# Performance work log

Hardware: AMD Instinct MI355X
Metric: run time of the kernel (lower is better)

The kernel has to match this reference:

```python
import jax, jax.numpy as jnp
import numpy as np

B, L, D = 128, 196, 512
T = 20
V, E, H, A = 10000, 256, 512, 512


def setup_inputs() -> dict:
    key = jax.random.key(0)
    ks = jax.random.split(key, 20)
    s = lambda *sh: 0.02
    inp = {
        "a": jax.random.normal(ks[0], (B, L, D), jnp.float32),
        "captions": jax.random.randint(ks[1], (B, T), 0, V),
        "lengths": jnp.full((B,), T, dtype=jnp.int64),
        "embed_W": jax.random.normal(ks[2], (V, E), jnp.float32) * 0.02,
        "Wa": jax.random.normal(ks[3], (D, A), jnp.float32) * 0.02,
        "Wh": jax.random.normal(ks[4], (H, A), jnp.float32) * 0.02,
        "Wc": jax.random.normal(ks[5], (H, A), jnp.float32) * 0.02,
        "v": jax.random.normal(ks[6], (A,), jnp.float32) * 0.02,
        "beta_W": jax.random.normal(ks[7], (H, 1), jnp.float32) * 0.02,
        "beta_b": jnp.zeros((1,), jnp.float32),
        "W_ih": jax.random.normal(ks[8], (E + D, 4 * H), jnp.float32) * 0.02,
        "W_hh": jax.random.normal(ks[9], (H, 4 * H), jnp.float32) * 0.02,
        "b_ih": jnp.zeros((4 * H,), jnp.float32),
        "b_hh": jnp.zeros((4 * H,), jnp.float32),
        "fc_W": jax.random.normal(ks[10], (H, V), jnp.float32) * 0.02,
        "fc_b": jnp.zeros((V,), jnp.float32),
        "initW_h": jax.random.normal(ks[11], (D, H), jnp.float32) * 0.02,
        "initb_h": jnp.zeros((H,), jnp.float32),
        "initW_c": jax.random.normal(ks[12], (D, H), jnp.float32) * 0.02,
        "initb_c": jnp.zeros((H,), jnp.float32),
    }
    return inp


def _decode(a, captions, embed_W, Wa, Wh, Wc, v, beta_W, beta_b,
            W_ih, W_hh, b_ih, b_hh, fc_W, fc_b,
            initW_h, initb_h, initW_c, initb_c):
    # dropout layers are treated as identity (eval mode) for a deterministic reference
    emb = embed_W[captions]                       # (B, T, E)
    mean_ctx = a.mean(axis=1)                     # (B, D)
    h0 = jnp.tanh(mean_ctx @ initW_h + initb_h)   # (B, H)
    c0 = jnp.tanh(mean_ctx @ initW_c + initb_c)
    wa = a @ Wa                                   # (B, L, A), hoisted (invariant over t)
    Hd = h0.shape[-1]

    def step(carry, x_t):
        h, c, prev_h = carry
        # dual additive attention: scores from annotations + h + prev_h (context_input)
        score = jnp.tanh(wa + (h @ Wh)[:, None, :] + (prev_h @ Wc)[:, None, :])  # (B,L,A)
        e = score @ v                                                            # (B,L)
        alpha = jax.nn.softmax(e, axis=1)
        beta = jax.nn.sigmoid(h @ beta_W + beta_b)                               # (B,1)
        ctx = beta * jnp.einsum('bl,bld->bd', alpha, a)                          # (B,D)
        # LSTMCell
        x = jnp.concatenate([x_t, ctx], axis=1)                                  # (B,E+D)
        gates = x @ W_ih + b_ih + h @ W_hh + b_hh                                # (B,4H)
        i, f, g, o = jnp.split(gates, 4, axis=1)
        c_new = jax.nn.sigmoid(f) * c + jax.nn.sigmoid(i) * jnp.tanh(g)
        h_new = jax.nn.sigmoid(o) * jnp.tanh(c_new)
        logits_t = h_new @ fc_W + fc_b                                           # (B,V)
        return (h_new, c_new, h_new), (logits_t, alpha)

    xs = jnp.swapaxes(emb[:, :T - 1, :], 0, 1)    # (T-1, B, E) time-major
    _, (logits_t, alphas_t) = jax.lax.scan(step, (h0, c0, h0), xs)
    # all lengths == T: pack_padded_sequence(batch_first=True).data is time-major flatten
    packed_logits = logits_t.reshape((T - 1) * a.shape[0], -1)                   # ((T-1)*B, V)
    alphas = jnp.swapaxes(alphas_t, 0, 1)                                        # (B, T-1, L)
    return packed_logits, alphas


def reference(a, captions, lengths, embed_W, Wa, Wh, Wc, v, beta_W, beta_b,
              W_ih, W_hh, b_ih, b_hh, fc_W, fc_b,
              initW_h, initb_h, initW_c, initb_c):
    return _decode(a, captions, embed_W, Wa, Wh, Wc, v, beta_W, beta_b,
                   W_ih, W_hh, b_ih, b_hh, fc_W, fc_b,
                   initW_h, initb_h, initW_c, initb_c)
```

## Files before the change

### kernel.cpp

```cpp
#include <hip/hip_runtime.h>
#include <hip/hip_bf16.h>
#include <math.h>

#define B_ 128
#define L_ 196
#define D_ 512
#define T_ 20
#define V_ 10000
#define E_ 256
#define H_ 512
#define A_ 512
#define TM1 19
#define ROWS (TM1*B_)
#define G4H 2048
#define KCAT 1024
#define LH 98

typedef unsigned short ushort_t;
typedef __attribute__((ext_vector_type(8))) short bf16x8;
typedef __attribute__((ext_vector_type(4))) float f32x4;

__device__ __forceinline__ float fast_tanh(float x){
    float ax = fabsf(x);
    float e = __expf(-2.f*ax);
    float r = __builtin_amdgcn_rcpf(1.f + e);
    return copysignf((1.f - e)*r, x);
}
__device__ __forceinline__ float sigmoidf_(float x){
    return __builtin_amdgcn_rcpf(1.f + __expf(-x));
}
__device__ __forceinline__ ushort_t f2b(float f){
    union{float f; unsigned u;} x; x.f = f;
    unsigned r = x.u + 0x7fffu + ((x.u>>16)&1u);
    return (ushort_t)(r>>16);
}
__device__ __forceinline__ float b2f(ushort_t h){
    union{unsigned u; float f;} x; x.u = ((unsigned)h)<<16;
    return x.f;
}
__device__ __forceinline__ float b2f_lo(unsigned u){ union{unsigned u; float f;} x; x.u = u<<16; return x.f; }
__device__ __forceinline__ float b2f_hi(unsigned u){ union{unsigned u; float f;} x; x.u = u & 0xffff0000u; return x.f; }

#define GL16(gsrc, ldst) __builtin_amdgcn_global_load_lds( \
    (const __attribute__((address_space(1))) unsigned*)(gsrc), \
    (__attribute__((address_space(3))) unsigned*)(ldst), 16, 0, 0)

template<int OUT_BF16, int HAS_BIAS, int NT, int SWZ>
__global__ __launch_bounds__(256)
void gemm_mfma(const ushort_t* __restrict__ A, int lda,
               const ushort_t* __restrict__ BT, int ldb,
               void* __restrict__ Cout, int ldc,
               int N, int K, const float* __restrict__ bias)
{
    __shared__ ushort_t As[2][4096];
    __shared__ ushort_t Bs[2][4096];
    int bm, bn;
    if (SWZ){
        int bid = blockIdx.x;
        int swz = (bid & 7)*190 + (bid >> 3);
        int mt = swz % 19, nt = swz / 19;
        if (nt >= 79) return;
        bm = mt*128; bn = nt*128;
    } else {
        bm = blockIdx.y * 128; bn = blockIdx.x * 128;
    }
    const int tid = threadIdx.x;
    const int lane = tid & 63;
    const int wave = tid >> 6;
    const int wm = (wave >> 1) * 64;
    const int wn = (wave & 1) * 64;
    const int lrow = lane & 15;
    const int lk8  = (lane >> 4) * 8;
    const int srow = tid >> 2;
    const int skq0 = (tid & 3) * 8;
    const int wbase = wave * 512;

    f32x4 acc[4][4];
    #pragma unroll
    for (int i=0;i<4;i++)
        #pragma unroll
        for (int j=0;j<4;j++) acc[i][j] = (f32x4){0.f,0.f,0.f,0.f};

    const ushort_t* Ab = A  + (size_t)(bm+srow)*lda + skq0;
    const ushort_t* Bb = BT + (size_t)(bn+srow)*ldb + skq0;

    GL16(Ab,                    &As[0][wbase]);
    GL16(Ab + (size_t)64*lda,   &As[0][2048 + wbase]);
    GL16(Bb,                    &Bs[0][wbase]);
    GL16(Bb + (size_t)64*ldb,   &Bs[0][2048 + wbase]);

    int buf = 0;
    for (int k0 = 0; k0 < K; k0 += 32) {
        asm volatile("s_waitcnt vmcnt(0)" ::: "memory");
        __syncthreads();
        if (k0 + 32 < K){
            int nb = buf ^ 1;
            GL16(Ab + k0 + 32,                  &As[nb][wbase]);
            GL16(Ab + (size_t)64*lda + k0 + 32, &As[nb][2048 + wbase]);
            GL16(Bb + k0 + 32,                  &Bs[nb][wbase]);
            GL16(Bb + (size_t)64*ldb + k0 + 32, &Bs[nb][2048 + wbase]);
        }
        bf16x8 af[4], bfr[4];
        #pragma unroll
        for (int i=0;i<4;i++) af[i]  = *(bf16x8*)&As[buf][(wm + i*16 + lrow)*32 + lk8];
        #pragma unroll
        for (int j=0;j<4;j++) bfr[j] = *(bf16x8*)&Bs[buf][(wn + j*16 + lrow)*32 + lk8];
        #pragma unroll
        for (int i=0;i<4;i++)
            #pragma unroll
            for (int j=0;j<4;j++)
                acc[i][j] = __builtin_amdgcn_mfma_f32_16x16x32_bf16(af[i], bfr[j], acc[i][j], 0, 0, 0);
        buf ^= 1;
    }

    const int rq = (lane >> 4) * 4;
    #pragma unroll
    for (int j=0;j<4;j++){
        int col = bn + wn + j*16 + lrow;
        if (col >= N) continue;
        float bv = HAS_BIAS ? bias[col] : 0.f;
        #pragma unroll
        for (int i=0;i<4;i++){
            #pragma unroll
            for (int q=0;q<4;q++){
                int row = bm + wm + i*16 + rq + q;
                float v = acc[i][j][q] + bv;
                if (OUT_BF16) ((ushort_t*)Cout)[(size_t)row*ldc + col] = f2b(v);
                else if (NT)  __builtin_nontemporal_store(v, &((float*)Cout)[(size_t)row*ldc + col]);
                else          ((float*)Cout)[(size_t)row*ldc + col] = v;
            }
        }
    }
}

struct GJob { const ushort_t* A; int lda; const ushort_t* BT; int ldb;
              void* C; int ldc; int N, K; const float* bias; int out_bf16; int nx; int nblk; };

__global__ __launch_bounds__(256) void gemm_dual_k(GJob j0, GJob j1){
    __shared__ ushort_t As[2][4096];
    __shared__ ushort_t Bs[2][4096];
    int bid = blockIdx.x;
    GJob jb = (bid < j0.nblk) ? j0 : j1;
    if (bid >= j0.nblk) bid -= j0.nblk;
    const int bn = (bid % jb.nx)*128, bm = (bid / jb.nx)*128;
    const int tid = threadIdx.x;
    const int lane = tid & 63;
    const int wave = tid >> 6;
    const int wm = (wave >> 1) * 64;
    const int wn = (wave & 1) * 64;
    const int lrow = lane & 15;
    const int lk8  = (lane >> 4) * 8;
    const int srow = tid >> 2;
    const int skq0 = (tid & 3) * 8;
    const int wbase = wave * 512;

    f32x4 acc[4][4];
    #pragma unroll
    for (int i=0;i<4;i++)
        #pragma unroll
        for (int j=0;j<4;j++) acc[i][j] = (f32x4){0.f,0.f,0.f,0.f};

    const ushort_t* Ab = jb.A  + (size_t)(bm+srow)*jb.lda + skq0;
    const ushort_t* Bb = jb.BT + (size_t)(bn+srow)*jb.ldb + skq0;

    GL16(Ab,                        &As[0][wbase]);
    GL16(Ab + (size_t)64*jb.lda,    &As[0][2048 + wbase]);
    GL16(Bb,                        &Bs[0][wbase]);
    GL16(Bb + (size_t)64*jb.ldb,    &Bs[0][2048 + wbase]);

    int buf = 0;
    for (int k0 = 0; k0 < jb.K; k0 += 32) {
        asm volatile("s_waitcnt vmcnt(0)" ::: "memory");
        __syncthreads();
        if (k0 + 32 < jb.K){
            int nb = buf ^ 1;
            GL16(Ab + k0 + 32,                      &As[nb][wbase]);
            GL16(Ab + (size_t)64*jb.lda + k0 + 32,  &As[nb][2048 + wbase]);
            GL16(Bb + k0 + 32,                      &Bs[nb][wbase]);
            GL16(Bb + (size_t)64*jb.ldb + k0 + 32,  &Bs[nb][2048 + wbase]);
        }
        bf16x8 af[4], bfr[4];
        #pragma unroll
        for (int i=0;i<4;i++) af[i]  = *(bf16x8*)&As[buf][(wm + i*16 + lrow)*32 + lk8];
        #pragma unroll
        for (int j=0;j<4;j++) bfr[j] = *(bf16x8*)&Bs[buf][(wn + j*16 + lrow)*32 + lk8];
        #pragma unroll
        for (int i=0;i<4;i++)
            #pragma unroll
            for (int j=0;j<4;j++)
                acc[i][j] = __builtin_amdgcn_mfma_f32_16x16x32_bf16(af[i], bfr[j], acc[i][j], 0, 0, 0);
        buf ^= 1;
    }

    const int rq = (lane >> 4) * 4;
    #pragma unroll
    for (int j=0;j<4;j++){
        int col = bn + wn + j*16 + lrow;
        if (col >= jb.N) continue;
        float bv = jb.bias ? jb.bias[col] : 0.f;
        #pragma unroll
        for (int i=0;i<4;i++){
            #pragma unroll
            for (int q=0;q<4;q++){
                int row = bm + wm + i*16 + rq + q;
                float v = acc[i][j][q] + bv;
                if (jb.out_bf16) ((ushort_t*)jb.C)[(size_t)row*jb.ldc + col] = f2b(v);
                else             ((float*)jb.C)[(size_t)row*jb.ldc + col] = v;
            }
        }
    }
}

__global__ __launch_bounds__(256) void gemm64t2(const float* __restrict__ Amcp, int lda,
                       const float* __restrict__ B0, const float* __restrict__ B1, int ldb,
                       float* __restrict__ C0, float* __restrict__ C1, int ldc,
                       const float* __restrict__ bias0, const float* __restrict__ bias1)
{
    const float* Bm  = blockIdx.z ? B1 : B0;
    float* C         = blockIdx.z ? C1 : C0;
    const float* bias= blockIdx.z ? bias1 : bias0;
    __shared__ float As[16][65];
    __shared__ float Bs[16][65];
    int bm = blockIdx.y*64, bn = blockIdx.x*64;
    int tid = threadIdx.x;
    int tx = tid & 15, ty = tid >> 4;
    const float invL = 1.f/(float)L_;
    float acc[4][4] = {};
    for (int k0 = 0; k0 < D_; k0 += 16) {
        {
            int r  = tid >> 2;
            int kq = (tid & 3) * 4;
            const float* Ap = Amcp + (size_t)(bm+r)*lda + k0 + kq;
            float4 v0 = *(const float4*)(Ap);
            float4 v1 = *(const float4*)(Ap + 65536);
            float4 v2 = *(const float4*)(Ap + 131072);
            float4 v3 = *(const float4*)(Ap + 196608);
            float4 va = make_float4((v0.x+v1.x+v2.x+v3.x)*invL, (v0.y+v1.y+v2.y+v3.y)*invL,
                                    (v0.z+v1.z+v2.z+v3.z)*invL, (v0.w+v1.w+v2.w+v3.w)*invL);
            As[kq+0][r]=va.x; As[kq+1][r]=va.y; As[kq+2][r]=va.z; As[kq+3][r]=va.w;
        }
        {
            int kk = tid >> 4;
            int nq = (tid & 15) * 4;
            float4 vb = *(const float4*)(Bm + (size_t)(k0+kk)*ldb + bn + nq);
            Bs[kk][nq+0]=vb.x; Bs[kk][nq+1]=vb.y; Bs[kk][nq+2]=vb.z; Bs[kk][nq+3]=vb.w;
        }
        __syncthreads();
        #pragma unroll
        for (int k = 0; k < 16; ++k) {
            float a0[4], b0[4];
            #pragma unroll
            for (int i=0;i<4;i++) a0[i] = As[k][ty*4+i];
            #pragma unroll
            for (int j=0;j<4;j++) b0[j] = Bs[k][tx*4+j];
            #pragma unroll
            for (int i=0;i<4;i++)
                #pragma unroll
                for (int j=0;j<4;j++)
                    acc[i][j] = fmaf(a0[i], b0[j], acc[i][j]);
        }
        __syncthreads();
    }
    #pragma unroll
    for (int i=0;i<4;i++){
        int row = bm + ty*4 + i;
        #pragma unroll
        for (int j=0;j<4;j++){
            int col = bn + tx*4 + j;
            C[(size_t)row*ldc + col] = fast_tanh(acc[i][j] + bias[col]);
        }
    }
}

struct TJob { const float* src; const float* src2; ushort_t* dst;
              int lds, Ksz, Nsz, koff, ldk, nx, nblk; };
struct PrepArgs {
    TJob j[6];
    const float* a; ushort_t* a_b; float* mcp;
    const float* b_ih; const float* b_hh; float* bias4h; unsigned* ebar;
    const int* caps; const float* embW; ushort_t* xemb;
};

__global__ __launch_bounds__(256) void prep_all_k(PrepArgs P){
    __shared__ float t[32][33];
    int bid = blockIdx.x;
    const int tid = threadIdx.x;
    if (bid < 256){
        const int b = bid >> 1, half = bid & 1;
        const int quad = tid & 127;
        const int sl = tid >> 7;
        const int pi = half*2 + sl;
        const int l0 = half*LH + sl*49;
        const float* p = P.a + ((size_t)(b*L_ + l0))*D_ + quad*4;
        ushort_t* q = P.a_b + ((size_t)(b*L_ + l0))*D_ + quad*4;
        float4 s = make_float4(0.f,0.f,0.f,0.f);
        for (int l=0;l<49;l++){
            float4 v = *(const float4*)(p + (size_t)l*D_);
            s.x += v.x; s.y += v.y; s.z += v.z; s.w += v.w;
            ushort_t r[4] = {f2b(v.x),f2b(v.y),f2b(v.z),f2b(v.w)};
            *(uint2*)(q + (size_t)l*D_) = *(uint2*)r;
        }
        *(float4*)(P.mcp + (size_t)pi*65536 + (size_t)b*D_ + quad*4) = s;
        return;
    }
    bid -= 256;
    if (bid < 8128){
        int ji = 0;
        while (bid >= P.j[ji].nblk){ bid -= P.j[ji].nblk; ji++; }
        const TJob jb = P.j[ji];
        int n0 = (bid % jb.nx)*32, k0 = (bid / jb.nx)*32;
        int tx = tid & 31, ty = tid >> 5;
        #pragma unroll
        for (int kk = ty; kk < 32; kk += 8){
            int k = k0 + kk, n = n0 + tx;
            float v = 0.f;
            if (k < jb.Ksz && n < jb.Nsz){
                v = jb.src[(size_t)k*jb.lds + n];
                if (jb.src2) v += jb.src2[(size_t)k*jb.lds + n];
            }
            t[kk][tx] = v;
        }
        __syncthreads();
        #pragma unroll
        for (int nn = ty; nn < 32; nn += 8){
            int n = n0 + nn, k = k0 + tx;
            if (k < jb.Ksz) jb.dst[(size_t)n*jb.ldk + jb.koff + k] = f2b(t[tx][nn]);
        }
        return;
    }
    bid -= 8128;
    if (bid == 0){
        for (int k = tid; k < G4H; k += 256) P.bias4h[k] = P.b_ih[k] + P.b_hh[k];
        if (tid < B_) P.ebar[tid] = 0u;
        return;
    }
    bid -= 1;
    int i = bid*4 + (tid >> 6);
    int lane = tid & 63;
    int tt = i / B_, b = i - tt*B_;
    int cap = P.caps[b*T_ + tt];
    float4 v = ((const float4*)(P.embW + (size_t)cap*E_))[lane];
    ushort_t r[4] = {f2b(v.x),f2b(v.y),f2b(v.z),f2b(v.w)};
    *(uint2*)(P.xemb + (size_t)i*E_ + lane*4) = *(uint2*)r;
}

__global__ __launch_bounds__(512) void hw0cvt_k(const float* __restrict__ h0f,
                        const ushort_t* __restrict__ WhcT, const float* __restrict__ beta_W,
                        ushort_t* __restrict__ xcat, float* __restrict__ hWp, float* __restrict__ bdot){
    int b = blockIdx.x, tid = threadIdx.x;
    int lane = tid & 63, wave = tid >> 6;
    __shared__ ushort_t hls[512];
    __shared__ float rr[8];
    float hv = h0f[b*H_ + tid];
    ushort_t hb = f2b(hv);
    xcat[(size_t)b*KCAT + D_ + tid] = hb;
    hls[tid] = hb;
    hWp[(size_t)(b*2+1)*512 + tid] = 0.f;
    float dv = hv * beta_W[tid];
    #pragma unroll
    for (int off=32; off; off>>=1) dv += __shfl_down(dv, off);
    if (lane==0) rr[wave] = dv;
    __syncthreads();
    if (tid == 0){
        float s = rr[0]+rr[1]+rr[2]+rr[3]+rr[4]+rr[5]+rr[6]+rr[7];
        bdot[b*2] = s; bdot[b*2+1] = 0.f;
    }
    int wn = wave * 64;
    int col16 = lane & 15;
    int khi = (lane >> 4) * 8;
    bool a_on = (col16 == 0);
    f32x4 acc[4];
    #pragma unroll
    for (int f=0;f<4;f++) acc[f] = (f32x4){0.f,0.f,0.f,0.f};
    for (int kk=0; kk<16; kk++){
        bf16x8 af = (bf16x8){0,0,0,0,0,0,0,0};
        if (a_on) af = *(const bf16x8*)&hls[kk*32 + khi];
        #pragma unroll
        for (int f=0;f<4;f++){
            bf16x8 bf = *(const bf16x8*)(WhcT + (size_t)(wn + f*16 + col16)*512 + kk*32 + khi);
            acc[f] = __builtin_amdgcn_mfma_f32_16x16x32_bf16(af, bf, acc[f], 0, 0, 0);
        }
    }
    if (lane < 16){
        #pragma unroll
        for (int f=0;f<4;f++) hWp[(size_t)(b*2+0)*512 + wn + f*16 + lane] = acc[f][0];
    }
}

__global__ __launch_bounds__(512) void mega2_k(const ushort_t* __restrict__ wa,
                        const ushort_t* __restrict__ a_b,
                        const float* __restrict__ v,
                        const float* __restrict__ beta_W, const float* __restrict__ beta_b,
                        const ushort_t* __restrict__ WhcT,
                        const float* __restrict__ gp, const float* __restrict__ embWih,
                        float* __restrict__ cbuf, float* __restrict__ hWp,
                        ushort_t* __restrict__ xcat, ushort_t* __restrict__ Hall,
                        float* __restrict__ alphas_out, float* __restrict__ ebuf,
                        unsigned* __restrict__ ebar, float* __restrict__ bdot, int t)
{
    const int b = blockIdx.x, half = blockIdx.y;
    const int tid = threadIdx.x;
    const int lane = tid & 63, wave = tid >> 6;
    __shared__ ushort_t hls[256];
    __shared__ float red[16];
    __shared__ float al_s[224];
    __shared__ float4 part4[8][64];

    if (t > 0){
        float dv = 0.f;
        if (tid < 256){
            const int j = half*256 + tid;
            const float* eb = embWih + ((size_t)((t-1)*B_ + b))*G4H;
            float gi = eb[j], gf = eb[H_+j], gg = eb[2*H_+j], go = eb[3*H_+j];
            #pragma unroll
            for (int ks=0; ks<8; ks++){
                const float* g = gp + ((size_t)(ks*B_ + b))*G4H;
                gi += g[j]; gf += g[H_+j]; gg += g[2*H_+j]; go += g[3*H_+j];
            }
            float ig = sigmoidf_(gi), fg = sigmoidf_(gf);
            float g2 = fast_tanh(gg), og = sigmoidf_(go);
            float c = fg*cbuf[b*H_+j] + ig*g2;
            float h = og*fast_tanh(c);
            cbuf[b*H_+j] = c;
            ushort_t hb = f2b(h);
            xcat[(size_t)b*KCAT + D_ + j] = hb;
            Hall[((size_t)(t-1)*B_ + b)*H_ + j] = hb;
            hls[tid] = hb;
            dv = h * beta_W[j];
        }
        #pragma unroll
        for (int off=32; off; off>>=1) dv += __shfl_down(dv, off);
        if (lane==0) red[wave] = dv;
        __syncthreads();
        int wn = wave * 64;
        int col16 = lane & 15;
        int khi = (lane >> 4) * 8;
        bool a_on = (col16 == 0);
        f32x4 acc[4];
        #pragma unroll
        for (int f=0;f<4;f++) acc[f] = (f32x4){0.f,0.f,0.f,0.f};
        #pragma unroll
        for (int kk=0; kk<8; kk++){
            bf16x8 af = (bf16x8){0,0,0,0,0,0,0,0};
            if (a_on) af = *(const bf16x8*)&hls[kk*32 + khi];
            #pragma unroll
            for (int f=0;f<4;f++){
                bf16x8 bf = *(const bf16x8*)(WhcT + (size_t)(wn + f*16 + col16)*512 + half*256 + kk*32 + khi);
                acc[f] = __builtin_amdgcn_mfma_f32_16x16x32_bf16(af, bf, acc[f], 0, 0, 0);
            }
        }
        if (lane < 16){
            #pragma unroll
            for (int f=0;f<4;f++) hWp[(size_t)(b*2+half)*512 + wn + f*16 + lane] = acc[f][0];
        }
    }
    __syncthreads();
    if (tid == 0){
        if (t > 0) bdot[b*2+half] = red[0]+red[1]+red[2]+red[3];
        __threadfence();
        atomicAdd(&ebar[b], 1u);
        const unsigned tgt = 2u*(unsigned)(2*t+1);
        while (__hip_atomic_load(&ebar[b], __ATOMIC_ACQUIRE, __HIP_MEMORY_SCOPE_AGENT) < tgt)
            __builtin_amdgcn_s_sleep(1);
    }
    __syncthreads();
    {
        const float* hp0 = hWp + (size_t)(b*2+0)*512 + lane*8;
        const float* hp1 = hWp + (size_t)(b*2+1)*512 + lane*8;
        float4 p00 = *(const float4*)hp0, p01 = *(const float4*)(hp0+4);
        float4 p10 = *(const float4*)hp1, p11 = *(const float4*)(hp1+4);
        float4 hw0 = make_float4(p00.x+p10.x, p00.y+p10.y, p00.z+p10.z, p00.w+p10.w);
        float4 hw1 = make_float4(p01.x+p11.x, p01.y+p11.y, p01.z+p11.z, p01.w+p11.w);
        const float* vp = v + lane*8;
        float4 v0 = *(const float4*)vp, v1 = *(const float4*)(vp+4);
        const int l0 = half*LH;
        for (int r = wave; r < LH; r += 8){
            int4 raw = *(const int4*)(wa + (((size_t)(b*L_ + l0 + r))<<9) + lane*8);
            const unsigned* u = (const unsigned*)&raw;
            float s;
            s  = fast_tanh(b2f_lo(u[0]) + hw0.x)*v0.x;
            s += fast_tanh(b2f_hi(u[0]) + hw0.y)*v0.y;
            s += fast_tanh(b2f_lo(u[1]) + hw0.z)*v0.z;
            s += fast_tanh(b2f_hi(u[1]) + hw0.w)*v0.w;
            s += fast_tanh(b2f_lo(u[2]) + hw1.x)*v1.x;
            s += fast_tanh(b2f_hi(u[2]) + hw1.y)*v1.y;
            s += fast_tanh(b2f_lo(u[3]) + hw1.z)*v1.z;
            s += fast_tanh(b2f_hi(u[3]) + hw1.w)*v1.w;
            #pragma unroll
            for (int off=32; off; off>>=1) s += __shfl_down(s, off);
            if (lane==0) ebuf[b*L_ + l0 + r] = s;
        }
    }
    __syncthreads();
    if (tid == 0){
        __threadfence();
        atomicAdd(&ebar[b], 1u);
        const unsigned tgt = 2u*(unsigned)(2*t+2);
        while (__hip_atomic_load(&ebar[b], __ATOMIC_ACQUIRE, __HIP_MEMORY_SCOPE_AGENT) < tgt)
            __builtin_amdgcn_s_sleep(1);
    }
    __syncthreads();
    float ev = (tid < L_) ? ebuf[b*L_ + tid] : -3.0e38f;
    float wmax = ev;
    #pragma unroll
    for (int off=32; off; off>>=1) wmax = fmaxf(wmax, __shfl_down(wmax, off));
    if (lane==0) red[wave] = wmax;
    __syncthreads();
    float m = fmaxf(fmaxf(fmaxf(red[0],red[1]),fmaxf(red[2],red[3])),
                    fmaxf(fmaxf(red[4],red[5]),fmaxf(red[6],red[7])));
    float pr = (tid < L_) ? __expf(ev - m) : 0.f;
    float wsum = pr;
    #pragma unroll
    for (int off=32; off; off>>=1) wsum += __shfl_down(wsum, off);
    if (lane==0) red[8+wave] = wsum;
    __syncthreads();
    float inv = 1.f / (red[8]+red[9]+red[10]+red[11]+red[12]+red[13]+red[14]+red[15]);
    if (tid < L_) al_s[tid] = pr*inv;
    const int l0 = half*LH;
    if (tid >= l0 && tid < l0 + LH)
        __builtin_nontemporal_store(pr*inv, alphas_out + (size_t)b*TM1*L_ + (size_t)t*L_ + tid);
    __syncthreads();
    {
        const int dg = tid & 63;
        const int lr = tid >> 6;
        const int d0 = half*256 + dg*4;
        const ushort_t* pa = a_b + (((size_t)(b*L_))<<9) + d0;
        float4 s = make_float4(0.f,0.f,0.f,0.f);
        for (int l = lr; l < L_; l += 8){
            uint2 av = *(const uint2*)(pa + ((size_t)l<<9));
            float al = al_s[l];
            s.x = fmaf(al, b2f_lo(av.x), s.x);
            s.y = fmaf(al, b2f_hi(av.x), s.y);
            s.z = fmaf(al, b2f_lo(av.y), s.z);
            s.w = fmaf(al, b2f_hi(av.y), s.w);
        }
        part4[lr][dg] = s;
        __syncthreads();
        if (tid < 64){
            float beta = sigmoidf_(bdot[b*2] + bdot[b*2+1] + beta_b[0]);
            float4 r = make_float4(0.f,0.f,0.f,0.f);
            #pragma unroll
            for (int q=0;q<8;q++){
                float4 pv = part4[q][tid];
                r.x += pv.x; r.y += pv.y; r.z += pv.z; r.w += pv.w;
            }
            unsigned lo = (unsigned)f2b(beta*r.x) | (((unsigned)f2b(beta*r.y))<<16);
            unsigned hi = (unsigned)f2b(beta*r.z) | (((unsigned)f2b(beta*r.w))<<16);
            uint2 pk; pk.x = lo; pk.y = hi;
            *(uint2*)(xcat + (size_t)b*KCAT + half*256 + tid*4) = pk;
        }
    }
}

__global__ __launch_bounds__(256) void gates_k(const ushort_t* __restrict__ xcat,
                        const ushort_t* __restrict__ WcatT, float* __restrict__ gp){
    __shared__ ushort_t As[128*32];
    __shared__ ushort_t Bs[64*32];
    const int bn = blockIdx.x*64;
    const int ks = blockIdx.y;
    const int tid = threadIdx.x;
    const int lane = tid & 63, wave = tid >> 6;
    const int wm = wave*32;
    const int lrow = lane & 15;
    const int lk8 = (lane >> 4) * 8;
    f32x4 acc[2][4];
    #pragma unroll
    for (int i=0;i<2;i++)
        #pragma unroll
        for (int j=0;j<4;j++) acc[i][j] = (f32x4){0.f,0.f,0.f,0.f};

    for (int kk = 0; kk < 4; ++kk){
        int k0 = ks*128 + kk*32;
        int c0 = 2*tid;
        int r0 = c0 >> 2,  kq0 = (c0 & 3)*8;
        int r1 = (c0+1) >> 2, kq1 = ((c0+1) & 3)*8;
        int4 a0 = *(const int4*)(xcat + (size_t)r0*KCAT + k0 + kq0);
        int4 a1 = *(const int4*)(xcat + (size_t)r1*KCAT + k0 + kq1);
        int rb = tid >> 2, kqb = (tid & 3)*8;
        int4 b0 = *(const int4*)(WcatT + (size_t)(bn+rb)*KCAT + k0 + kqb);
        __syncthreads();
        *(int4*)&As[r0*32 + kq0] = a0;
        *(int4*)&As[r1*32 + kq1] = a1;
        *(int4*)&Bs[rb*32 + kqb] = b0;
        __syncthreads();
        bf16x8 af[2], bfr[4];
        #pragma unroll
        for (int i=0;i<2;i++) af[i] = *(bf16x8*)&As[(wm + i*16 + lrow)*32 + lk8];
        #pragma unroll
        for (int j=0;j<4;j++) bfr[j] = *(bf16x8*)&Bs[(j*16 + lrow)*32 + lk8];
        #pragma unroll
        for (int i=0;i<2;i++)
            #pragma unroll
            for (int j=0;j<4;j++)
                acc[i][j] = __builtin_amdgcn_mfma_f32_16x16x32_bf16(af[i], bfr[j], acc[i][j], 0, 0, 0);
    }
    const int rq = (lane >> 4) * 4;
    #pragma unroll
    for (int i=0;i<2;i++){
        #pragma unroll
        for (int j=0;j<4;j++){
            int gcol = bn + j*16 + lrow;
            #pragma unroll
            for (int q=0;q<4;q++){
                int grow = wm + i*16 + rq + q;
                gp[((size_t)(ks*B_ + grow))*G4H + gcol] = acc[i][j][q];
            }
        }
    }
}

__global__ __launch_bounds__(512) void lstmfin_k(const float* __restrict__ gp, const float* __restrict__ embWih,
                       const float* __restrict__ cbuf, ushort_t* __restrict__ Hall){
    int b = blockIdx.x, j = threadIdx.x;
    const float* eb = embWih + ((size_t)(18*B_ + b))*G4H;
    float gi = eb[j], gf = eb[H_+j], gg = eb[2*H_+j], go = eb[3*H_+j];
    #pragma unroll
    for (int ks=0; ks<8; ks++){
        const float* g = gp + ((size_t)(ks*B_ + b))*G4H;
        gi += g[j]; gf += g[H_+j]; gg += g[2*H_+j]; go += g[3*H_+j];
    }
    float ig = sigmoidf_(gi), fg = sigmoidf_(gf);
    float g2 = fast_tanh(gg), og = sigmoidf_(go);
    float c = fg*cbuf[b*H_+j] + ig*g2;
    float h = og*fast_tanh(c);
    Hall[((size_t)18*B_ + b)*H_ + j] = f2b(h);
}

extern "C" void kernel_launch(void* const* d_in, const int* in_sizes, int n_in,
                              void* d_out, int out_size, void* d_ws, size_t ws_size,
                              hipStream_t stream) {
    const float* a      = (const float*)d_in[0];
    const int*   caps   = (const int*)  d_in[1];
    const float* embW   = (const float*)d_in[3];
    const float* Wa     = (const float*)d_in[4];
    const float* Wh     = (const float*)d_in[5];
    const float* Wc     = (const float*)d_in[6];
    const float* v      = (const float*)d_in[7];
    const float* beta_W = (const float*)d_in[8];
    const float* beta_b = (const float*)d_in[9];
    const float* W_ih   = (const float*)d_in[10];
    const float* W_hh   = (const float*)d_in[11];
    const float* b_ih   = (const float*)d_in[12];
    const float* b_hh   = (const float*)d_in[13];
    const float* fc_W   = (const float*)d_in[14];
    const float* fc_b   = (const float*)d_in[15];
    const float* iWh    = (const float*)d_in[16];
    const float* ibh    = (const float*)d_in[17];
    const float* iWc    = (const float*)d_in[18];
    const float* ibc    = (const float*)d_in[19];

    float* out    = (float*)d_out;
    float* alphas = out + (size_t)ROWS*V_;

    char* ob = (char*)d_out;
    ushort_t* wa_b   = (ushort_t*)(ob);
    ushort_t* a_b    = (ushort_t*)(ob + 25690112);
    float*    embWih = (float*)   (ob + 51380224);

    char* wb = (char*)d_ws;
    float* mcp      = (float*)(wb);
    float* bdot     = (float*)(wb + 1048576);
    float* cbuf     = (float*)(wb + 1052672);
    float* h0f      = (float*)(wb + 1314816);
    float* hWp      = (float*)(wb + 1576960);
    float* ebuf     = (float*)(wb + 2101248);
    float* bias4h   = (float*)(wb + 2203648);
    unsigned* ebar  = (unsigned*)(wb + 2211840);
    float* gp       = (float*)(wb + 2215936);
    ushort_t* xcat_b = (ushort_t*)(wb + 10604544);
    ushort_t* xemb_b = (ushort_t*)(wb + 10866688);
    ushort_t* Hall   = (ushort_t*)(wb + 12111872);
    ushort_t* WaT    = (ushort_t*)(wb + 14602240);
    ushort_t* WhcT   = (ushort_t*)(wb + 15126528);
    ushort_t* WihT   = (ushort_t*)(wb + 15650816);
    ushort_t* WcatT  = (ushort_t*)(wb + 16699392);
    ushort_t* fcWT   = (ushort_t*)(wb + 20893696);

    PrepArgs P;
    P.j[0] = { Wa,   nullptr, WaT,  512, 512, 512,  0,   512,  16, 256 };
    P.j[1] = { Wh,   Wc,      WhcT, 512, 512, 512,  0,   512,  16, 256 };
    P.j[2] = { W_ih, nullptr, WihT, G4H, 256, G4H,  0,   256,  64, 512 };
    P.j[3] = { W_ih + (size_t)E_*G4H, nullptr, WcatT, G4H, 512, G4H, 0,   KCAT, 64, 1024 };
    P.j[4] = { W_hh, nullptr, WcatT, G4H, 512, G4H,  512, KCAT, 64, 1024 };
    P.j[5] = { fc_W, nullptr, fcWT, V_,  512, V_,   0,   512,  316, 5056 };
    P.a = a; P.a_b = a_b; P.mcp = mcp;
    P.b_ih = b_ih; P.b_hh = b_hh; P.bias4h = bias4h; P.ebar = ebar;
    P.caps = caps; P.embW = embW; P.xemb = xemb_b;
    prep_all_k<<<8993, 256, 0, stream>>>(P);

    gemm64t2<<<dim3(8,2,2), 256, 0, stream>>>(mcp, D_, iWh, iWc, H_, h0f, cbuf, H_, ibh, ibc);
    hw0cvt_k<<<B_, 512, 0, stream>>>(h0f, WhcT, beta_W, xcat_b, hWp, bdot);

    GJob g0 = { a_b,    512, WaT,  512, wa_b,   512, 512,  512, nullptr, 1, 4,  784 };
    GJob g1 = { xemb_b, 256, WihT, 256, embWih, G4H, G4H,  256, bias4h,  0, 16, 304 };
    gemm_dual_k<<<1088, 256, 0, stream>>>(g0, g1);

    for (int t = 0; t < TM1; ++t){
        mega2_k<<<dim3(B_,2), 512, 0, stream>>>(wa_b, a_b, v, beta_W, beta_b, WhcT,
                                                gp, embWih, cbuf, hWp, xcat_b, Hall,
                                                alphas, ebuf, ebar, bdot, t);
        gates_k<<<dim3(32,8), 256, 0, stream>>>(xcat_b, WcatT, gp);
    }
    lstmfin_k<<<B_, 512, 0, stream>>>(gp, embWih, cbuf, Hall);

    gemm_mfma<0,1,1,1><<<dim3(1520), 256, 0, stream>>>(Hall, H_, fcWT, H_, out, V_, V_, H_, fc_b);
}
```

Measured before the change: 1.062 ms.

## Fuse gates GEMM into per-step attention kernel via grid-wide barrier

Merges the per-timestep gates GEMM into the attention/LSTM kernel. A software grid barrier (an atomic counter on a global word plus spin-wait) lets all 256 blocks finish writing xcat before any block computes its gates tile. This removes 19 kernel launches and their launch gaps, and reuses the same blocks for the GEMM with a reworked wave tiling. It relies on all 256 blocks being co-resident, otherwise the spin-wait deadlocks, and it adds LDS usage to the fused kernel.

```diff
diff --git a/kernel.cpp b/kernel.cpp
--- a/kernel.cpp
+++ b/kernel.cpp
@@ -277,7 +277,7 @@
 struct PrepArgs {
     TJob j[6];
     const float* a; ushort_t* a_b; float* mcp;
-    const float* b_ih; const float* b_hh; float* bias4h; unsigned* ebar;
+    const float* b_ih; const float* b_hh; float* bias4h; unsigned* bars;
     const int* caps; const float* embW; ushort_t* xemb;
 };
 
@@ -331,7 +331,7 @@
     bid -= 8128;
     if (bid == 0){
         for (int k = tid; k < G4H; k += 256) P.bias4h[k] = P.b_ih[k] + P.b_hh[k];
-        if (tid < B_) P.ebar[tid] = 0u;
+        P.bars[tid] = 0u;
         return;
     }
     bid -= 1;
@@ -387,24 +387,29 @@
     }
 }
 
-__global__ __launch_bounds__(512) void mega2_k(const ushort_t* __restrict__ wa,
+__global__ __launch_bounds__(512) void mega_k(const ushort_t* __restrict__ wa,
                         const ushort_t* __restrict__ a_b,
                         const float* __restrict__ v,
                         const float* __restrict__ beta_W, const float* __restrict__ beta_b,
-                        const ushort_t* __restrict__ WhcT,
-                        const float* __restrict__ gp, const float* __restrict__ embWih,
+                        const ushort_t* __restrict__ WhcT, const ushort_t* __restrict__ WcatT,
+                        const float* __restrict__ embWih,
                         float* __restrict__ cbuf, float* __restrict__ hWp,
                         ushort_t* __restrict__ xcat, ushort_t* __restrict__ Hall,
                         float* __restrict__ alphas_out, float* __restrict__ ebuf,
-                        unsigned* __restrict__ ebar, float* __restrict__ bdot, int t)
+                        float* __restrict__ gp,
+                        unsigned* __restrict__ ebar, unsigned* __restrict__ gbar,
+                        float* __restrict__ bdot, int t)
 {
-    const int b = blockIdx.x, half = blockIdx.y;
+    const int blk = blockIdx.x;
+    const int b = blk >> 1, half = blk & 1;
     const int tid = threadIdx.x;
     const int lane = tid & 63, wave = tid >> 6;
     __shared__ ushort_t hls[256];
     __shared__ float red[16];
     __shared__ float al_s[224];
     __shared__ float4 part4[8][64];
+    __shared__ ushort_t As[128*32];
+    __shared__ ushort_t Bs[64*32];
 
     if (t > 0){
         float dv = 0.f;
@@ -550,62 +555,60 @@
             *(uint2*)(xcat + (size_t)b*KCAT + half*256 + tid*4) = pk;
         }
     }
-}
-
-__global__ __launch_bounds__(256) void gates_k(const ushort_t* __restrict__ xcat,
-                        const ushort_t* __restrict__ WcatT, float* __restrict__ gp){
-    __shared__ ushort_t As[128*32];
-    __shared__ ushort_t Bs[64*32];
-    const int bn = blockIdx.x*64;
-    const int ks = blockIdx.y;
-    const int tid = threadIdx.x;
-    const int lane = tid & 63, wave = tid >> 6;
-    const int wm = wave*32;
-    const int lrow = lane & 15;
-    const int lk8 = (lane >> 4) * 8;
-    f32x4 acc[2][4];
-    #pragma unroll
-    for (int i=0;i<2;i++)
-        #pragma unroll
-        for (int j=0;j<4;j++) acc[i][j] = (f32x4){0.f,0.f,0.f,0.f};
-
-    for (int kk = 0; kk < 4; ++kk){
-        int k0 = ks*128 + kk*32;
-        int c0 = 2*tid;
-        int r0 = c0 >> 2,  kq0 = (c0 & 3)*8;
-        int r1 = (c0+1) >> 2, kq1 = ((c0+1) & 3)*8;
-        int4 a0 = *(const int4*)(xcat + (size_t)r0*KCAT + k0 + kq0);
-        int4 a1 = *(const int4*)(xcat + (size_t)r1*KCAT + k0 + kq1);
-        int rb = tid >> 2, kqb = (tid & 3)*8;
-        int4 b0 = *(const int4*)(WcatT + (size_t)(bn+rb)*KCAT + k0 + kqb);
-        __syncthreads();
-        *(int4*)&As[r0*32 + kq0] = a0;
-        *(int4*)&As[r1*32 + kq1] = a1;
-        *(int4*)&Bs[rb*32 + kqb] = b0;
-        __syncthreads();
-        bf16x8 af[2], bfr[4];
-        #pragma unroll
-        for (int i=0;i<2;i++) af[i] = *(bf16x8*)&As[(wm + i*16 + lrow)*32 + lk8];
-        #pragma unroll
-        for (int j=0;j<4;j++) bfr[j] = *(bf16x8*)&Bs[(j*16 + lrow)*32 + lk8];
+    __syncthreads();
+    if (tid == 0){
+        __threadfence();
+        atomicAdd(gbar, 1u);
+        const unsigned tgt = 256u*(unsigned)(t+1);
+        while (__hip_atomic_load(gbar, __ATOMIC_ACQUIRE, __HIP_MEMORY_SCOPE_AGENT) < tgt)
+            __builtin_amdgcn_s_sleep(1);
+    }
+    __syncthreads();
+    {
+        const int bn = (blk & 31) * 64;
+        const int ks = blk >> 5;
+        const int wm = (wave & 3) * 32;
+        const int wn = (wave >> 2) * 32;
+        const int lrow = lane & 15, lk8 = (lane >> 4) * 8;
+        const int ra = tid >> 2, kqa = (tid & 3)*8;
+        f32x4 acc[2][2];
         #pragma unroll
         for (int i=0;i<2;i++)
             #pragma unroll
-            for (int j=0;j<4;j++)
-                acc[i][j] = __builtin_amdgcn_mfma_f32_16x16x32_bf16(af[i], bfr[j], acc[i][j], 0, 0, 0);
-    }
-    const int rq = (lane >> 4) * 4;
-    #pragma unroll
-    for (int i=0;i<2;i++){
-        #pragma unroll
-        for (int j=0;j<4;j++){
-            int gcol = bn + j*16 + lrow;
-            #pragma unroll
-            for (int q=0;q<4;q++){
-                int grow = wm + i*16 + rq + q;
-                gp[((size_t)(ks*B_ + grow))*G4H + gcol] = acc[i][j][q];
+            for (int j=0;j<2;j++) acc[i][j] = (f32x4){0.f,0.f,0.f,0.f};
+        #pragma unroll
+        for (int kk = 0; kk < 4; ++kk){
+            int k0 = ks*128 + kk*32;
+            int4 av = *(const int4*)(xcat + (size_t)ra*KCAT + k0 + kqa);
+            int4 bv;
+            if (tid < 256) bv = *(const int4*)(WcatT + (size_t)(bn + ra)*KCAT + k0 + kqa);
+            __syncthreads();
+            *(int4*)&As[ra*32 + kqa] = av;
+            if (tid < 256) *(int4*)&Bs[ra*32 + kqa] = bv;
+            __syncthreads();
+            bf16x8 af[2], bfr[2];
+            #pragma unroll
+            for (int i=0;i<2;i++) af[i]  = *(bf16x8*)&As[(wm + i*16 + lrow)*32 + lk8];
+            #pragma unroll
+            for (int j=0;j<2;j++) bfr[j] = *(bf16x8*)&Bs[(wn + j*16 + lrow)*32 + lk8];
+            #pragma unroll
+            for (int i=0;i<2;i++)
+                #pragma unroll
+                for (int j=0;j<2;j++)
+                    acc[i][j] = __builtin_amdgcn_mfma_f32_16x16x32_bf16(af[i], bfr[j], acc[i][j], 0, 0, 0);
+        }
+        const int rq = (lane >> 4) * 4;
+        #pragma unroll
+        for (int i=0;i<2;i++)
+            #pragma unroll
+            for (int j=0;j<2;j++){
+                int gcol = bn + wn + j*16 + lrow;
+                #pragma unroll
+                for (int q=0;q<4;q++){
+                    int grow = wm + i*16 + rq + q;
+                    gp[((size_t)(ks*B_ + grow))*G4H + gcol] = acc[i][j][q];
+                }
             }
-        }
     }
 }
 
@@ -665,7 +668,7 @@
     float* hWp      = (float*)(wb + 1576960);
     float* ebuf     = (float*)(wb + 2101248);
     float* bias4h   = (float*)(wb + 2203648);
-    unsigned* ebar  = (unsigned*)(wb + 2211840);
+    unsigned* bars  = (unsigned*)(wb + 2211840);
     float* gp       = (float*)(wb + 2215936);
     ushort_t* xcat_b = (ushort_t*)(wb + 10604544);
     ushort_t* xemb_b = (ushort_t*)(wb + 10866688);
@@ -684,7 +687,7 @@
     P.j[4] = { W_hh, nullptr, WcatT, G4H, 512, G4H,  512, KCAT, 64, 1024 };
     P.j[5] = { fc_W, nullptr, fcWT, V_,  512, V_,   0,   512,  316, 5056 };
     P.a = a; P.a_b = a_b; P.mcp = mcp;
-    P.b_ih = b_ih; P.b_hh = b_hh; P.bias4h = bias4h; P.ebar = ebar;
+    P.b_ih = b_ih; P.b_hh = b_hh; P.bias4h = bias4h; P.bars = bars;
     P.caps = caps; P.embW = embW; P.xemb = xemb_b;
     prep_all_k<<<8993, 256, 0, stream>>>(P);
 
@@ -696,10 +699,9 @@
     gemm_dual_k<<<1088, 256, 0, stream>>>(g0, g1);
 
     for (int t = 0; t < TM1; ++t){
-        mega2_k<<<dim3(B_,2), 512, 0, stream>>>(wa_b, a_b, v, beta_W, beta_b, WhcT,
-                                                gp, embWih, cbuf, hWp, xcat_b, Hall,
-                                                alphas, ebuf, ebar, bdot, t);
-        gates_k<<<dim3(32,8), 256, 0, stream>>>(xcat_b, WcatT, gp);
+        mega_k<<<256, 512, 0, stream>>>(wa_b, a_b, v, beta_W, beta_b, WhcT, WcatT,
+                                        embWih, cbuf, hWp, xcat_b, Hall,
+                                        alphas, ebuf, gp, bars, bars + 128, bdot, t);
     }
     lstmfin_k<<<B_, 512, 0, stream>>>(gp, embWih, cbuf, Hall);
 
```

New measurement: 1.440 ms. 1.36x slower.

## Stage logits epilogue through LDS for vector stores; double mega2 block size

Applied to the files above, without the earlier changes.

The final logits GEMM epilogue now writes accumulators into shared memory in 32-row chunks and then emits coalesced 16-byte nontemporal stores with a vectorized bias add, in place of scattered scalar stores. The per-step attention kernel mega2_k moves from 512 to 1024 threads per block, halving per-wave loop trip counts and widening the reductions to 16 waves. The aim is better write coalescing on the large logits output and more parallelism per recurrent step, at the cost of extra barriers and LDS traffic in the epilogue and higher register pressure under the 1024-thread launch bound. The barrier-array initialization also changes to clear 256 entries.

```diff
diff --git a/kernel.cpp b/kernel.cpp
--- a/kernel.cpp
+++ b/kernel.cpp
@@ -45,25 +45,19 @@
     (const __attribute__((address_space(1))) unsigned*)(gsrc), \
     (__attribute__((address_space(3))) unsigned*)(ldst), 16, 0, 0)
 
-template<int OUT_BF16, int HAS_BIAS, int NT, int SWZ>
 __global__ __launch_bounds__(256)
-void gemm_mfma(const ushort_t* __restrict__ A, int lda,
-               const ushort_t* __restrict__ BT, int ldb,
-               void* __restrict__ Cout, int ldc,
-               int N, int K, const float* __restrict__ bias)
+void gemm_logits_k(const ushort_t* __restrict__ A, int lda,
+                   const ushort_t* __restrict__ BT, int ldb,
+                   float* __restrict__ C, int ldc,
+                   int N, int K, const float* __restrict__ bias)
 {
     __shared__ ushort_t As[2][4096];
     __shared__ ushort_t Bs[2][4096];
-    int bm, bn;
-    if (SWZ){
-        int bid = blockIdx.x;
-        int swz = (bid & 7)*190 + (bid >> 3);
-        int mt = swz % 19, nt = swz / 19;
-        if (nt >= 79) return;
-        bm = mt*128; bn = nt*128;
-    } else {
-        bm = blockIdx.y * 128; bn = blockIdx.x * 128;
-    }
+    int bid = blockIdx.x;
+    int swz = (bid & 7)*190 + (bid >> 3);
+    int mt = swz % 19, nt = swz / 19;
+    if (nt >= 79) return;
+    const int bm = mt*128, bn = nt*128;
     const int tid = threadIdx.x;
     const int lane = tid & 63;
     const int wave = tid >> 6;
@@ -114,20 +108,39 @@
     }
 
     const int rq = (lane >> 4) * 4;
-    #pragma unroll
-    for (int j=0;j<4;j++){
-        int col = bn + wn + j*16 + lrow;
-        if (col >= N) continue;
-        float bv = HAS_BIAS ? bias[col] : 0.f;
-        #pragma unroll
-        for (int i=0;i<4;i++){
-            #pragma unroll
-            for (int q=0;q<4;q++){
-                int row = bm + wm + i*16 + rq + q;
-                float v = acc[i][j][q] + bv;
-                if (OUT_BF16) ((ushort_t*)Cout)[(size_t)row*ldc + col] = f2b(v);
-                else if (NT)  __builtin_nontemporal_store(v, &((float*)Cout)[(size_t)row*ldc + col]);
-                else          ((float*)Cout)[(size_t)row*ldc + col] = v;
+    float* eps = (float*)As;
+    #pragma unroll
+    for (int c = 0; c < 4; ++c){
+        __syncthreads();
+        if ((wave >> 1) == (c >> 1)){
+            const int ib = 2*(c & 1);
+            #pragma unroll
+            for (int ii = 0; ii < 2; ++ii){
+                #pragma unroll
+                for (int j = 0; j < 4; ++j){
+                    #pragma unroll
+                    for (int q = 0; q < 4; ++q){
+                        int lr_ = ii*16 + rq + q;
+                        int lc  = wn + j*16 + lrow;
+                        eps[lr_*128 + lc] = acc[ib+ii][j][q];
+                    }
+                }
+            }
+        }
+        __syncthreads();
+        for (int it = tid; it < 1024; it += 256){
+            int r = it >> 5, c4 = it & 31;
+            int col0 = bn + c4*4;
+            if (col0 >= N) continue;
+            f32x4 vv = *(f32x4*)&eps[r*128 + c4*4];
+            float* dst = &C[(size_t)(bm + 32*c + r)*ldc + col0];
+            if (col0 + 3 < N){
+                float4 bb = *(const float4*)(bias + col0);
+                vv[0] += bb.x; vv[1] += bb.y; vv[2] += bb.z; vv[3] += bb.w;
+                __builtin_nontemporal_store(vv, (f32x4*)dst);
+            } else {
+                for (int e=0; e<4 && col0+e < N; ++e)
+                    __builtin_nontemporal_store(vv[e] + bias[col0+e], dst + e);
             }
         }
     }
@@ -277,7 +290,7 @@
 struct PrepArgs {
     TJob j[6];
     const float* a; ushort_t* a_b; float* mcp;
-    const float* b_ih; const float* b_hh; float* bias4h; unsigned* ebar;
+    const float* b_ih; const float* b_hh; float* bias4h; unsigned* bars;
     const int* caps; const float* embW; ushort_t* xemb;
 };
 
@@ -331,7 +344,7 @@
     bid -= 8128;
     if (bid == 0){
         for (int k = tid; k < G4H; k += 256) P.bias4h[k] = P.b_ih[k] + P.b_hh[k];
-        if (tid < B_) P.ebar[tid] = 0u;
+        P.bars[tid] = 0u;
         return;
     }
     bid -= 1;
@@ -387,7 +400,7 @@
     }
 }
 
-__global__ __launch_bounds__(512) void mega2_k(const ushort_t* __restrict__ wa,
+__global__ __launch_bounds__(1024) void mega2_k(const ushort_t* __restrict__ wa,
                         const ushort_t* __restrict__ a_b,
                         const float* __restrict__ v,
                         const float* __restrict__ beta_W, const float* __restrict__ beta_b,
@@ -402,9 +415,9 @@
     const int tid = threadIdx.x;
     const int lane = tid & 63, wave = tid >> 6;
     __shared__ ushort_t hls[256];
-    __shared__ float red[16];
+    __shared__ float red[32];
     __shared__ float al_s[224];
-    __shared__ float4 part4[8][64];
+    __shared__ float4 part4[16][64];
 
     if (t > 0){
         float dv = 0.f;
@@ -432,31 +445,36 @@
         for (int off=32; off; off>>=1) dv += __shfl_down(dv, off);
         if (lane==0) red[wave] = dv;
         __syncthreads();
-        int wn = wave * 64;
+        int wn = wave * 32;
         int col16 = lane & 15;
         int khi = (lane >> 4) * 8;
         bool a_on = (col16 == 0);
-        f32x4 acc[4];
-        #pragma unroll
-        for (int f=0;f<4;f++) acc[f] = (f32x4){0.f,0.f,0.f,0.f};
+        f32x4 acc[2];
+        acc[0] = (f32x4){0.f,0.f,0.f,0.f};
+        acc[1] = (f32x4){0.f,0.f,0.f,0.f};
         #pragma unroll
         for (int kk=0; kk<8; kk++){
             bf16x8 af = (bf16x8){0,0,0,0,0,0,0,0};
             if (a_on) af = *(const bf16x8*)&hls[kk*32 + khi];
             #pragma unroll
-            for (int f=0;f<4;f++){
+            for (int f=0;f<2;f++){
                 bf16x8 bf = *(const bf16x8*)(WhcT + (size_t)(wn + f*16 + col16)*512 + half*256 + kk*32 + khi);
                 acc[f] = __builtin_amdgcn_mfma_f32_16x16x32_bf16(af, bf, acc[f], 0, 0, 0);
             }
         }
         if (lane < 16){
             #pragma unroll
-            for (int f=0;f<4;f++) hWp[(size_t)(b*2+half)*512 + wn + f*16 + lane] = acc[f][0];
+            for (int f=0;f<2;f++) hWp[(size_t)(b*2+half)*512 + wn + f*16 + lane] = acc[f][0];
         }
     }
     __syncthreads();
     if (tid == 0){
-        if (t > 0) bdot[b*2+half] = red[0]+red[1]+red[2]+red[3];
+        if (t > 0){
+            float s = 0.f;
+            #pragma unroll
+            for (int w=0; w<16; w++) s += red[w];
+            bdot[b*2+half] = s;
+        }
         __threadfence();
         atomicAdd(&ebar[b], 1u);
         const unsigned tgt = 2u*(unsigned)(2*t+1);
@@ -474,7 +492,7 @@
         const float* vp = v + lane*8;
         float4 v0 = *(const float4*)vp, v1 = *(const float4*)(vp+4);
         const int l0 = half*LH;
-        for (int r = wave; r < LH; r += 8){
+        for (int r = wave; r < LH; r += 16){
             int4 raw = *(const int4*)(wa + (((size_t)(b*L_ + l0 + r))<<9) + lane*8);
             const unsigned* u = (const unsigned*)&raw;
             float s;
@@ -506,15 +524,19 @@
     for (int off=32; off; off>>=1) wmax = fmaxf(wmax, __shfl_down(wmax, off));
     if (lane==0) red[wave] = wmax;
     __syncthreads();
-    float m = fmaxf(fmaxf(fmaxf(red[0],red[1]),fmaxf(red[2],red[3])),
-                    fmaxf(fmaxf(red[4],red[5]),fmaxf(red[6],red[7])));
+    float m = red[0];
+    #pragma unroll
+    for (int w=1; w<16; w++) m = fmaxf(m, red[w]);
     float pr = (tid < L_) ? __expf(ev - m) : 0.f;
     float wsum = pr;
     #pragma unroll
     for (int off=32; off; off>>=1) wsum += __shfl_down(wsum, off);
-    if (lane==0) red[8+wave] = wsum;
+    if (lane==0) red[16+wave] = wsum;
     __syncthreads();
-    float inv = 1.f / (red[8]+red[9]+red[10]+red[11]+red[12]+red[13]+red[14]+red[15]);
+    float sum = red[16];
+    #pragma unroll
+    for (int w=1; w<16; w++) sum += red[16+w];
+    float inv = 1.f / sum;
     if (tid < L_) al_s[tid] = pr*inv;
     const int l0 = half*LH;
     if (tid >= l0 && tid < l0 + LH)
@@ -526,7 +548,7 @@
         const int d0 = half*256 + dg*4;
         const ushort_t* pa = a_b + (((size_t)(b*L_))<<9) + d0;
         float4 s = make_float4(0.f,0.f,0.f,0.f);
-        for (int l = lr; l < L_; l += 8){
+        for (int l = lr; l < L_; l += 16){
             uint2 av = *(const uint2*)(pa + ((size_t)l<<9));
             float al = al_s[l];
             s.x = fmaf(al, b2f_lo(av.x), s.x);
@@ -540,7 +562,7 @@
             float beta = sigmoidf_(bdot[b*2] + bdot[b*2+1] + beta_b[0]);
             float4 r = make_float4(0.f,0.f,0.f,0.f);
             #pragma unroll
-            for (int q=0;q<8;q++){
+            for (int q=0;q<16;q++){
                 float4 pv = part4[q][tid];
                 r.x += pv.x; r.y += pv.y; r.z += pv.z; r.w += pv.w;
             }
@@ -665,7 +687,7 @@
     float* hWp      = (float*)(wb + 1576960);
     float* ebuf     = (float*)(wb + 2101248);
     float* bias4h   = (float*)(wb + 2203648);
-    unsigned* ebar  = (unsigned*)(wb + 2211840);
+    unsigned* bars  = (unsigned*)(wb + 2211840);
     float* gp       = (float*)(wb + 2215936);
     ushort_t* xcat_b = (ushort_t*)(wb + 10604544);
     ushort_t* xemb_b = (ushort_t*)(wb + 10866688);
@@ -684,7 +706,7 @@
     P.j[4] = { W_hh, nullptr, WcatT, G4H, 512, G4H,  512, KCAT, 64, 1024 };
     P.j[5] = { fc_W, nullptr, fcWT, V_,  512, V_,   0,   512,  316, 5056 };
     P.a = a; P.a_b = a_b; P.mcp = mcp;
-    P.b_ih = b_ih; P.b_hh = b_hh; P.bias4h = bias4h; P.ebar = ebar;
+    P.b_ih = b_ih; P.b_hh = b_hh; P.bias4h = bias4h; P.bars = bars;
     P.caps = caps; P.embW = embW; P.xemb = xemb_b;
     prep_all_k<<<8993, 256, 0, stream>>>(P);
 
@@ -696,12 +718,12 @@
     gemm_dual_k<<<1088, 256, 0, stream>>>(g0, g1);
 
     for (int t = 0; t < TM1; ++t){
-        mega2_k<<<dim3(B_,2), 512, 0, stream>>>(wa_b, a_b, v, beta_W, beta_b, WhcT,
-                                                gp, embWih, cbuf, hWp, xcat_b, Hall,
-                                                alphas, ebuf, ebar, bdot, t);
+        mega2_k<<<dim3(B_,2), 1024, 0, stream>>>(wa_b, a_b, v, beta_W, beta_b, WhcT,
+                                                 gp, embWih, cbuf, hWp, xcat_b, Hall,
+                                                 alphas, ebuf, bars, bdot, t);
         gates_k<<<dim3(32,8), 256, 0, stream>>>(xcat_b, WcatT, gp);
     }
     lstmfin_k<<<B_, 512, 0, stream>>>(gp, embWih, cbuf, Hall);
 
-    gemm_mfma<0,1,1,1><<<dim3(1520), 256, 0, stream>>>(Hall, H_, fcWT, H_, out, V_, V_, H_, fc_b);
-}
+    gemm_logits_k<<<dim3(1520), 256, 0, stream>>>(Hall, H_, fcWT, H_, out, V_, V_, H_, fc_b);
+}
```

After: 977.4 us. 8.0% less time.
